# Performance work log

Hardware: AMD Instinct MI355X
Metric: run time of the kernel (lower is better)

Reference implementation:

```python
import jax, jax.numpy as jnp
import numpy as np

B, L, D, H = 4, 1024, 1024, 16
HD = D // H  # head_dim = 64


def setup_inputs() -> dict:
    key = jax.random.key(0)
    k1, k2, k3, k4 = jax.random.split(key, 4)
    x = jax.random.normal(k1, (B, L, D), dtype=jnp.float32)
    # causal mask: positions where mask == 0 are filled with -inf
    mask = jnp.tril(jnp.ones((L, L), dtype=bool))[None, None, :, :]  # [1,1,L,L]
    w_qkv = jax.random.normal(k2, (D, 3 * D), dtype=jnp.float32) * (D ** -0.5)
    w_out = jax.random.normal(k3, (D, D), dtype=jnp.float32) * (D ** -0.5)
    rel_pos_bias = jax.random.normal(k4, (H, L, L), dtype=jnp.float32) * 0.02
    return {"x": x, "mask": mask, "w_qkv": w_qkv, "w_out": w_out,
            "rel_pos_bias": rel_pos_bias}


def reference(x, mask, w_qkv, w_out, rel_pos_bias):
    b, l, d = x.shape
    scale = HD ** -0.5
    qkv = (x @ w_qkv).reshape(b, l, 3, H, HD)          # [B,L,3,H,hd]
    q, k, v = qkv[:, :, 0], qkv[:, :, 1], qkv[:, :, 2]  # each [B,L,H,hd]
    # scores: [B,H,Lq,Lk]
    scores = jnp.einsum('bqhd,bkhd->bhqk', q, k) * scale
    scores = scores + rel_pos_bias[None, :, :l, :l]
    scores = jnp.where(mask, scores, -jnp.inf)
    attn = jax.nn.softmax(scores, axis=-1)  # dropout is identity in eval
    out = jnp.einsum('bhqk,bkhd->bqhd', attn, v).reshape(b, l, d)
    return out @ w_out
```

## Files before the change

kernel.cpp:

```cpp
#include <hip/hip_runtime.h>
#include <hip/hip_bf16.h>
#include <math.h>

#define B_  4
#define L_  1024
#define D_  1024
#define H_  16
#define HD_ 64
#define SCALE 0.125f
#define LOG2E 1.44269504f
#define SCALE_L2E (0.125f * 1.44269504f)
#define NEG_BIG -3.0e38f

typedef __bf16 bf16x8 __attribute__((ext_vector_type(8)));
typedef float  f32x4  __attribute__((ext_vector_type(4)));

__device__ __forceinline__ float b2f(unsigned short u) {
    union { unsigned int i; float f; } x; x.i = ((unsigned)u) << 16; return x.f;
}
__device__ __forceinline__ unsigned short f2b(float f) {
    __hip_bfloat16 h = __float2bfloat16(f);
    return *reinterpret_cast<unsigned short*>(&h);
}
__device__ __forceinline__ void gl_lds16(const void* g, void* l) {
    __builtin_amdgcn_global_load_lds(
        (const __attribute__((address_space(1))) void*)g,
        (__attribute__((address_space(3))) void*)l, 16, 0, 0);
}

__global__ __launch_bounds__(256) void prep_kernel(
    const float* __restrict__ x, const float* __restrict__ w_qkv,
    const float* __restrict__ w_out, unsigned short* __restrict__ xb,
    unsigned short* __restrict__ wqkvT, unsigned short* __restrict__ woutT)
{
    const int bid = blockIdx.x;
    if (bid < 4096) {
        int i = (bid * 256 + threadIdx.x) * 4;
        float4 v = *(const float4*)&x[i];
        ushort4 o = make_ushort4(f2b(v.x), f2b(v.y), f2b(v.z), f2b(v.w));
        *(ushort4*)&xb[i] = o;
        return;
    }
    __shared__ float tile[32][33];
    const float* w; unsigned short* wt; int N, n0, k0;
    if (bid < 7168) {
        int b2 = bid - 4096;
        w = w_qkv; wt = wqkvT; N = 3072;
        n0 = (b2 % 96) * 32; k0 = (b2 / 96) * 32;
    } else {
        int b3 = bid - 7168;
        w = w_out; wt = woutT; N = 1024;
        n0 = (b3 % 32) * 32; k0 = (b3 / 32) * 32;
    }
    const int tx = threadIdx.x & 31, ty = threadIdx.x >> 5;
#pragma unroll
    for (int i = 0; i < 4; i++) {
        int kk = ty + i * 8;
        tile[kk][tx] = w[(size_t)(k0 + kk) * N + n0 + tx];
    }
    __syncthreads();
#pragma unroll
    for (int i = 0; i < 4; i++) {
        int nn = ty + i * 8;
        wt[(size_t)(n0 + nn) * 1024 + k0 + tx] = f2b(tile[tx][nn]);
    }
}

__device__ __forceinline__ void gemm_core(
    const unsigned short* __restrict__ A, const unsigned short* __restrict__ Bt,
    unsigned short* As, unsigned short* Bs,
    int m0, int n0, int wave, int lane, int wm, int wn,
    f32x4 acc[4][4])
{
    const int srow = lane >> 2, spos = lane & 3;
    const int sc   = spos ^ ((srow >> 1) & 3);
    const int mlane = lane & 15, chunk = lane >> 4;
    const int foff  = mlane * 32 + (chunk ^ ((mlane >> 1) & 3)) * 8;

    for (int k0 = 0; k0 < 1024; k0 += 32) {
#pragma unroll
        for (int t = 0; t < 2; t++) {
            int rb = wave * 32 + t * 16;
            int r  = rb + srow;
            gl_lds16(&A [(size_t)(m0 + r) * 1024 + k0 + sc * 8], &As[rb * 32]);
            gl_lds16(&Bt[(size_t)(n0 + r) * 1024 + k0 + sc * 8], &Bs[rb * 32]);
        }
        __syncthreads();
        bf16x8 af[4], bfr[4];
#pragma unroll
        for (int i = 0; i < 4; i++) {
            af[i]  = *(const bf16x8*)&As[(wm * 64 + i * 16) * 32 + foff];
            bfr[i] = *(const bf16x8*)&Bs[(wn * 64 + i * 16) * 32 + foff];
        }
#pragma unroll
        for (int i = 0; i < 4; i++)
#pragma unroll
            for (int j = 0; j < 4; j++)
                acc[i][j] = __builtin_amdgcn_mfma_f32_16x16x32_bf16(
                    bfr[i], af[j], acc[i][j], 0, 0, 0);
        __syncthreads();
    }
}

__global__ __launch_bounds__(256) void qkv_gemm_kernel(
    const unsigned short* __restrict__ A, const unsigned short* __restrict__ Bt,
    unsigned short* __restrict__ qb, unsigned short* __restrict__ kb,
    unsigned short* __restrict__ vtb)
{
    __shared__ unsigned short As[128 * 32];
    __shared__ unsigned short Bs[128 * 32];
    const int tid  = threadIdx.x;
    const int wave = tid >> 6, lane = tid & 63;
    const int quad = lane >> 4, l16 = lane & 15;
    const int wm = wave >> 1, wn = wave & 1;
    const int m0 = blockIdx.y * 128, n0 = blockIdx.x * 128;
    f32x4 acc[4][4] = {};
    gemm_core(A, Bt, As, Bs, m0, n0, wave, lane, wm, wn, acc);

    const int s = n0 >> 10;
#pragma unroll
    for (int i = 0; i < 4; i++) {
        int n_base = n0 + wn * 64 + i * 16 + quad * 4;
        int h = (n_base >> 6) & 15, hd0 = n_base & 63;
#pragma unroll
        for (int j = 0; j < 4; j++) {
            int m = m0 + wm * 64 + j * 16 + l16;
            int b = m >> 10, l = m & 1023;
            if (s == 2) {
#pragma unroll
                for (int r = 0; r < 4; r++)
                    vtb[((size_t)((b * 16 + h) * 64 + hd0 + r)) * 1024 + l] =
                        f2b(acc[i][j][r]);
            } else {
                unsigned short* dst = (s == 0) ? qb : kb;
                unsigned short tmp[4];
#pragma unroll
                for (int r = 0; r < 4; r++) tmp[r] = f2b(acc[i][j][r]);
                *(ushort4*)&dst[(((size_t)(b * 16 + h) * 1024 + l) << 6) + hd0] =
                    *(ushort4*)tmp;
            }
        }
    }
}

__global__ __launch_bounds__(256) void out_gemm_kernel(
    const unsigned short* __restrict__ A, const unsigned short* __restrict__ Bt,
    float* __restrict__ out)
{
    __shared__ unsigned short As[128 * 32];
    __shared__ unsigned short Bs[64 * 32];
    const int tid  = threadIdx.x;
    const int wave = tid >> 6, lane = tid & 63;
    const int quad = lane >> 4, l16 = lane & 15;
    const int srow = lane >> 2, spos = lane & 3;
    const int sc   = spos ^ ((srow >> 1) & 3);
    const int mlane = lane & 15, chunk = lane >> 4;
    const int foff  = mlane * 32 + (chunk ^ ((mlane >> 1) & 3)) * 8;
    const int m0 = blockIdx.y * 128, n0 = blockIdx.x * 64;
    f32x4 acc[4][2] = {};

    for (int k0 = 0; k0 < 1024; k0 += 32) {
#pragma unroll
        for (int t = 0; t < 2; t++) {
            int rb = wave * 32 + t * 16;
            gl_lds16(&A[(size_t)(m0 + rb + srow) * 1024 + k0 + sc * 8], &As[rb * 32]);
        }
        {
            int rb = wave * 16;
            gl_lds16(&Bt[(size_t)(n0 + rb + srow) * 1024 + k0 + sc * 8], &Bs[rb * 32]);
        }
        __syncthreads();
        bf16x8 af[2], bfr[4];
#pragma unroll
        for (int i = 0; i < 2; i++)
            af[i]  = *(const bf16x8*)&As[(wave * 32 + i * 16) * 32 + foff];
#pragma unroll
        for (int j = 0; j < 4; j++)
            bfr[j] = *(const bf16x8*)&Bs[(j * 16) * 32 + foff];
#pragma unroll
        for (int jn = 0; jn < 4; jn++)
#pragma unroll
            for (int im = 0; im < 2; im++)
                acc[jn][im] = __builtin_amdgcn_mfma_f32_16x16x32_bf16(
                    bfr[jn], af[im], acc[jn][im], 0, 0, 0);
        __syncthreads();
    }
#pragma unroll
    for (int jn = 0; jn < 4; jn++) {
        int n_base = n0 + jn * 16 + quad * 4;
#pragma unroll
        for (int im = 0; im < 2; im++) {
            int m = m0 + wave * 32 + im * 16 + l16;
            float4 o = make_float4(acc[jn][im][0], acc[jn][im][1],
                                   acc[jn][im][2], acc[jn][im][3]);
            *(float4*)&out[(size_t)m * 1024 + n_base] = o;
        }
    }
}

__global__ __launch_bounds__(256, 4) void attn_mfma_kernel(
    const unsigned short* __restrict__ qb, const unsigned short* __restrict__ kb,
    const unsigned short* __restrict__ vtb, const float* __restrict__ bias,
    unsigned short* __restrict__ ob)
{
    __shared__ unsigned short Qs[64 * 72];
    __shared__ unsigned short Ks[64 * 72];
    __shared__ unsigned short Vts[64 * 72];
    __shared__ unsigned short Ps[64 * 72];

    const int tid  = threadIdx.x;
    const int wave = tid >> 6, lane = tid & 63;
    const int quad = lane >> 4, l16 = lane & 15;
    const int bh = blockIdx.x, b = bh >> 4, h = bh & 15;
    const int qt = blockIdx.y;
    const int q0 = qt * 64;
    const int srow = tid >> 3, scol = (tid & 7) * 8;
    const size_t qkv_base = (size_t)bh * (1024 * 64);
    const int qg_base = q0 + wave * 16 + quad * 4;

#pragma unroll
    for (int i = 0; i < 2; i++) {
        int r = srow + i * 32;
        *(uint4*)&Qs[r * 72 + scol] =
            *(const uint4*)&qb[qkv_base + (size_t)(q0 + r) * 64 + scol];
    }
    uint4 kpre0 = *(const uint4*)&kb[qkv_base + (size_t)srow * 64 + scol];
    uint4 kpre1 = *(const uint4*)&kb[qkv_base + (size_t)(srow + 32) * 64 + scol];
    uint4 vpre0 = *(const uint4*)&vtb[qkv_base + (size_t)srow * 1024 + scol];
    uint4 vpre1 = *(const uint4*)&vtb[qkv_base + (size_t)(srow + 32) * 1024 + scol];

    float bA[16], bB[16];
    {
        const float* bp0 = &bias[((size_t)h * 1024 + qg_base) * 1024];
#pragma unroll
        for (int nt = 0; nt < 4; nt++)
#pragma unroll
            for (int r = 0; r < 4; r++)
                bA[nt * 4 + r] = bp0[(size_t)r * 1024 + nt * 16 + l16] * LOG2E;
    }

    float l_run[4] = {0.f, 0.f, 0.f, 0.f};
    f32x4 Oacc[4] = {};

    __syncthreads();
    bf16x8 af0 = *(const bf16x8*)&Qs[(wave * 16 + l16) * 72 + quad * 8];
    bf16x8 af1 = *(const bf16x8*)&Qs[(wave * 16 + l16) * 72 + 32 + quad * 8];

    auto attn_tile = [&](int kt, float* bcur, float* bnxt) {
        const int k0 = kt * 64;
        *(uint4*)&Ks [(size_t)srow * 72 + scol]        = kpre0;
        *(uint4*)&Ks [(size_t)(srow + 32) * 72 + scol] = kpre1;
        *(uint4*)&Vts[(size_t)srow * 72 + scol]        = vpre0;
        *(uint4*)&Vts[(size_t)(srow + 32) * 72 + scol] = vpre1;
        __syncthreads();
        if (kt < qt) {
            const int kn = k0 + 64;
            kpre0 = *(const uint4*)&kb[qkv_base + (size_t)(kn + srow) * 64 + scol];
            kpre1 = *(const uint4*)&kb[qkv_base + (size_t)(kn + srow + 32) * 64 + scol];
            vpre0 = *(const uint4*)&vtb[qkv_base + (size_t)srow * 1024 + kn + scol];
            vpre1 = *(const uint4*)&vtb[qkv_base + (size_t)(srow + 32) * 1024 + kn + scol];
            const float* bp = &bias[((size_t)h * 1024 + qg_base) * 1024 + kn];
#pragma unroll
            for (int nt = 0; nt < 4; nt++)
#pragma unroll
                for (int r = 0; r < 4; r++)
                    bnxt[nt * 4 + r] = bp[(size_t)r * 1024 + nt * 16 + l16] * LOG2E;
        }
        f32x4 sacc[4] = {};
#pragma unroll
        for (int nt = 0; nt < 4; nt++) {
            bf16x8 bk0 = *(const bf16x8*)&Ks[(nt * 16 + l16) * 72 + quad * 8];
            bf16x8 bk1 = *(const bf16x8*)&Ks[(nt * 16 + l16) * 72 + 32 + quad * 8];
            sacc[nt] = __builtin_amdgcn_mfma_f32_16x16x32_bf16(af0, bk0, sacc[nt], 0, 0, 0);
            sacc[nt] = __builtin_amdgcn_mfma_f32_16x16x32_bf16(af1, bk1, sacc[nt], 0, 0, 0);
        }
        const bool diag = (kt == qt);
#pragma unroll
        for (int nt = 0; nt < 4; nt++) {
            const int kg = k0 + nt * 16 + l16;
#pragma unroll
            for (int r = 0; r < 4; r++) {
                float v = fmaf(sacc[nt][r], SCALE_L2E, bcur[nt * 4 + r]);
                if (diag && kg > qg_base + r) v = NEG_BIG;
                float p = exp2f(v);
                l_run[r] += p;
                Ps[(wave * 16 + quad * 4 + r) * 72 + nt * 16 + l16] = f2b(p);
            }
        }
        bf16x8 pf0 = *(const bf16x8*)&Ps[(wave * 16 + l16) * 72 + quad * 8];
        bf16x8 pf1 = *(const bf16x8*)&Ps[(wave * 16 + l16) * 72 + 32 + quad * 8];
#pragma unroll
        for (int dt = 0; dt < 4; dt++) {
            bf16x8 vf0 = *(const bf16x8*)&Vts[(dt * 16 + l16) * 72 + quad * 8];
            bf16x8 vf1 = *(const bf16x8*)&Vts[(dt * 16 + l16) * 72 + 32 + quad * 8];
            Oacc[dt] = __builtin_amdgcn_mfma_f32_16x16x32_bf16(pf0, vf0, Oacc[dt], 0, 0, 0);
            Oacc[dt] = __builtin_amdgcn_mfma_f32_16x16x32_bf16(pf1, vf1, Oacc[dt], 0, 0, 0);
        }
        __syncthreads();
    };

    for (int kt = 0; kt <= qt; kt += 2) {
        attn_tile(kt, bA, bB);
        if (kt + 1 <= qt) attn_tile(kt + 1, bB, bA);
    }

#pragma unroll
    for (int r = 0; r < 4; r++) {
        float s = l_run[r];
        s += __shfl_xor(s, 1);
        s += __shfl_xor(s, 2);
        s += __shfl_xor(s, 4);
        s += __shfl_xor(s, 8);
        float inv = 1.0f / s;
        int qg = qg_base + r;
#pragma unroll
        for (int dt = 0; dt < 4; dt++)
            ob[((size_t)(b * 1024 + qg)) * 1024 + h * 64 + dt * 16 + l16] =
                f2b(Oacc[dt][r] * inv);
    }
}


extern "C" void kernel_launch(void* const* d_in, const int* in_sizes, int n_in,
                              void* d_out, int out_size, void* d_ws, size_t ws_size,
                              hipStream_t stream) {
    const float* x     = (const float*)d_in[0];
    const float* w_qkv = (const float*)d_in[2];
    const float* w_out = (const float*)d_in[3];
    const float* bias  = (const float*)d_in[4];
    float* out = (float*)d_out;

    char* ws = (char*)d_ws;
    unsigned short* xb     = (unsigned short*)ws;              ws += (size_t)4096 * 1024 * 2;
    unsigned short* wqkvT  = (unsigned short*)ws;              ws += (size_t)3072 * 1024 * 2;
    unsigned short* woutT  = (unsigned short*)ws;              ws += (size_t)1024 * 1024 * 2;
    unsigned short* qb     = (unsigned short*)ws;              ws += (size_t)4096 * 1024 * 2;
    unsigned short* kb     = (unsigned short*)ws;              ws += (size_t)4096 * 1024 * 2;
    unsigned short* vtb    = (unsigned short*)ws;              ws += (size_t)4096 * 1024 * 2;
    unsigned short* ab     = (unsigned short*)ws;

    prep_kernel<<<8192, 256, 0, stream>>>(x, w_qkv, w_out, xb, wqkvT, woutT);
    qkv_gemm_kernel<<<dim3(24, 32), 256, 0, stream>>>(xb, wqkvT, qb, kb, vtb);
    attn_mfma_kernel<<<dim3(64, 16), 256, 0, stream>>>(qb, kb, vtb, bias, ab);
    out_gemm_kernel<<<dim3(16, 32), 256, 0, stream>>>(ab, woutT, out);
}
```

Baseline: 222.2 us.

## Pair causal query tiles per block for load balance with double-buffered K/V

Each attention block now handles two query tiles, jlo and 15-jlo, so every block does the same amount of causal work, and the grid is halved. K and V tiles are shared between the two query strips. K/V LDS tiles are double-buffered so the next tile is written after compute, needing one barrier per tile. Q fragments load straight from global into registers, and s_setprio raises priority around the MFMA sections. Occupancy bound drops to 2 blocks per CU, and register pressure grows from the two accumulator sets.

Measured after the change: 215.9 us. -2.8%, faster.

```diff
diff --git a/kernel.cpp b/kernel.cpp
--- a/kernel.cpp
+++ b/kernel.cpp
@@ -198,125 +198,163 @@
     }
 }
 
-__global__ __launch_bounds__(256, 4) void attn_mfma_kernel(
+__global__ __launch_bounds__(256, 2) void attn_mfma_kernel(
     const unsigned short* __restrict__ qb, const unsigned short* __restrict__ kb,
     const unsigned short* __restrict__ vtb, const float* __restrict__ bias,
     unsigned short* __restrict__ ob)
 {
-    __shared__ unsigned short Qs[64 * 72];
-    __shared__ unsigned short Ks[64 * 72];
-    __shared__ unsigned short Vts[64 * 72];
-    __shared__ unsigned short Ps[64 * 72];
+    __shared__ unsigned short Ks [2 * 64 * 72];
+    __shared__ unsigned short Vts[2 * 64 * 72];
+    __shared__ unsigned short Ps [128 * 72];
 
     const int tid  = threadIdx.x;
     const int wave = tid >> 6, lane = tid & 63;
     const int quad = lane >> 4, l16 = lane & 15;
     const int bh = blockIdx.x, b = bh >> 4, h = bh & 15;
-    const int qt = blockIdx.y;
-    const int q0 = qt * 64;
+    const int jlo = blockIdx.y;
+    const int jhi = 15 - jlo;
+    const int ktmax = jhi;
     const int srow = tid >> 3, scol = (tid & 7) * 8;
     const size_t qkv_base = (size_t)bh * (1024 * 64);
-    const int qg_base = q0 + wave * 16 + quad * 4;
-
-#pragma unroll
-    for (int i = 0; i < 2; i++) {
-        int r = srow + i * 32;
-        *(uint4*)&Qs[r * 72 + scol] =
-            *(const uint4*)&qb[qkv_base + (size_t)(q0 + r) * 64 + scol];
-    }
-    uint4 kpre0 = *(const uint4*)&kb[qkv_base + (size_t)srow * 64 + scol];
-    uint4 kpre1 = *(const uint4*)&kb[qkv_base + (size_t)(srow + 32) * 64 + scol];
+
+    const int qH  = jhi * 64 + wave * 16;
+    const int qL  = jlo * 64 + wave * 16;
+    const int qgH = qH + quad * 4;
+    const int qgL = qL + quad * 4;
+
+    bf16x8 aH0 = *(const bf16x8*)&qb[qkv_base + (size_t)(qH + l16) * 64 + quad * 8];
+    bf16x8 aH1 = *(const bf16x8*)&qb[qkv_base + (size_t)(qH + l16) * 64 + 32 + quad * 8];
+    bf16x8 aL0 = *(const bf16x8*)&qb[qkv_base + (size_t)(qL + l16) * 64 + quad * 8];
+    bf16x8 aL1 = *(const bf16x8*)&qb[qkv_base + (size_t)(qL + l16) * 64 + 32 + quad * 8];
+
+    uint4 kpre0 = *(const uint4*)&kb [qkv_base + (size_t)srow * 64 + scol];
+    uint4 kpre1 = *(const uint4*)&kb [qkv_base + (size_t)(srow + 32) * 64 + scol];
     uint4 vpre0 = *(const uint4*)&vtb[qkv_base + (size_t)srow * 1024 + scol];
     uint4 vpre1 = *(const uint4*)&vtb[qkv_base + (size_t)(srow + 32) * 1024 + scol];
 
     float bA[16], bB[16];
-    {
-        const float* bp0 = &bias[((size_t)h * 1024 + qg_base) * 1024];
-#pragma unroll
-        for (int nt = 0; nt < 4; nt++)
-#pragma unroll
-            for (int r = 0; r < 4; r++)
-                bA[nt * 4 + r] = bp0[(size_t)r * 1024 + nt * 16 + l16] * LOG2E;
-    }
-
-    float l_run[4] = {0.f, 0.f, 0.f, 0.f};
-    f32x4 Oacc[4] = {};
-
+#pragma unroll
+    for (int nt = 0; nt < 4; nt++)
+#pragma unroll
+        for (int r = 0; r < 4; r++)
+            bA[nt * 4 + r] =
+                bias[((size_t)h * 1024 + qgH + r) * 1024 + nt * 16 + l16] * LOG2E;
+
+    float lrH[4] = {}, lrL[4] = {};
+    f32x4 OH[4] = {}, OL[4] = {};
+
+    *(uint4*)&Ks [srow * 72 + scol]        = kpre0;
+    *(uint4*)&Ks [(srow + 32) * 72 + scol] = kpre1;
+    *(uint4*)&Vts[srow * 72 + scol]        = vpre0;
+    *(uint4*)&Vts[(srow + 32) * 72 + scol] = vpre1;
     __syncthreads();
-    bf16x8 af0 = *(const bf16x8*)&Qs[(wave * 16 + l16) * 72 + quad * 8];
-    bf16x8 af1 = *(const bf16x8*)&Qs[(wave * 16 + l16) * 72 + 32 + quad * 8];
-
-    auto attn_tile = [&](int kt, float* bcur, float* bnxt) {
-        const int k0 = kt * 64;
-        *(uint4*)&Ks [(size_t)srow * 72 + scol]        = kpre0;
-        *(uint4*)&Ks [(size_t)(srow + 32) * 72 + scol] = kpre1;
-        *(uint4*)&Vts[(size_t)srow * 72 + scol]        = vpre0;
-        *(uint4*)&Vts[(size_t)(srow + 32) * 72 + scol] = vpre1;
-        __syncthreads();
-        if (kt < qt) {
-            const int kn = k0 + 64;
-            kpre0 = *(const uint4*)&kb[qkv_base + (size_t)(kn + srow) * 64 + scol];
-            kpre1 = *(const uint4*)&kb[qkv_base + (size_t)(kn + srow + 32) * 64 + scol];
+
+    auto strip = [&](int kt, const bf16x8& a0, const bf16x8& a1, const float* bc,
+                     int qg, int psrow, f32x4* O, float* lr, bool dg) {
+        const unsigned short* Kc = &Ks [(kt & 1) * 4608];
+        const unsigned short* Vc = &Vts[(kt & 1) * 4608];
+        f32x4 sacc[4] = {};
+        __builtin_amdgcn_s_setprio(1);
+#pragma unroll
+        for (int nt = 0; nt < 4; nt++) {
+            bf16x8 k0 = *(const bf16x8*)&Kc[(nt * 16 + l16) * 72 + quad * 8];
+            bf16x8 k1 = *(const bf16x8*)&Kc[(nt * 16 + l16) * 72 + 32 + quad * 8];
+            sacc[nt] = __builtin_amdgcn_mfma_f32_16x16x32_bf16(a0, k0, sacc[nt], 0, 0, 0);
+            sacc[nt] = __builtin_amdgcn_mfma_f32_16x16x32_bf16(a1, k1, sacc[nt], 0, 0, 0);
+        }
+        __builtin_amdgcn_s_setprio(0);
+#pragma unroll
+        for (int nt = 0; nt < 4; nt++) {
+            const int kg = kt * 64 + nt * 16 + l16;
+#pragma unroll
+            for (int r = 0; r < 4; r++) {
+                float v = fmaf(sacc[nt][r], SCALE_L2E, bc[nt * 4 + r]);
+                if (dg && kg > qg + r) v = NEG_BIG;
+                float p = exp2f(v);
+                lr[r] += p;
+                Ps[(psrow + quad * 4 + r) * 72 + nt * 16 + l16] = f2b(p);
+            }
+        }
+        bf16x8 p0 = *(const bf16x8*)&Ps[(psrow + l16) * 72 + quad * 8];
+        bf16x8 p1 = *(const bf16x8*)&Ps[(psrow + l16) * 72 + 32 + quad * 8];
+        __builtin_amdgcn_s_setprio(1);
+#pragma unroll
+        for (int dt = 0; dt < 4; dt++) {
+            bf16x8 v0 = *(const bf16x8*)&Vc[(dt * 16 + l16) * 72 + quad * 8];
+            bf16x8 v1 = *(const bf16x8*)&Vc[(dt * 16 + l16) * 72 + 32 + quad * 8];
+            O[dt] = __builtin_amdgcn_mfma_f32_16x16x32_bf16(p0, v0, O[dt], 0, 0, 0);
+            O[dt] = __builtin_amdgcn_mfma_f32_16x16x32_bf16(p1, v1, O[dt], 0, 0, 0);
+        }
+        __builtin_amdgcn_s_setprio(0);
+    };
+
+    auto tile = [&](int kt, float* bc, float* bn) {
+        const bool pf = (kt < ktmax);
+        if (pf) {
+            const int kn = (kt + 1) * 64;
+            kpre0 = *(const uint4*)&kb [qkv_base + (size_t)(kn + srow) * 64 + scol];
+            kpre1 = *(const uint4*)&kb [qkv_base + (size_t)(kn + srow + 32) * 64 + scol];
             vpre0 = *(const uint4*)&vtb[qkv_base + (size_t)srow * 1024 + kn + scol];
             vpre1 = *(const uint4*)&vtb[qkv_base + (size_t)(srow + 32) * 1024 + kn + scol];
-            const float* bp = &bias[((size_t)h * 1024 + qg_base) * 1024 + kn];
+            const float* bp = &bias[((size_t)h * 1024 + qgH) * 1024 + kn];
 #pragma unroll
             for (int nt = 0; nt < 4; nt++)
 #pragma unroll
                 for (int r = 0; r < 4; r++)
-                    bnxt[nt * 4 + r] = bp[(size_t)r * 1024 + nt * 16 + l16] * LOG2E;
-        }
-        f32x4 sacc[4] = {};
-#pragma unroll
-        for (int nt = 0; nt < 4; nt++) {
-            bf16x8 bk0 = *(const bf16x8*)&Ks[(nt * 16 + l16) * 72 + quad * 8];
-            bf16x8 bk1 = *(const bf16x8*)&Ks[(nt * 16 + l16) * 72 + 32 + quad * 8];
-            sacc[nt] = __builtin_amdgcn_mfma_f32_16x16x32_bf16(af0, bk0, sacc[nt], 0, 0, 0);
-            sacc[nt] = __builtin_amdgcn_mfma_f32_16x16x32_bf16(af1, bk1, sacc[nt], 0, 0, 0);
-        }
-        const bool diag = (kt == qt);
-#pragma unroll
-        for (int nt = 0; nt < 4; nt++) {
-            const int kg = k0 + nt * 16 + l16;
-#pragma unroll
-            for (int r = 0; r < 4; r++) {
-                float v = fmaf(sacc[nt][r], SCALE_L2E, bcur[nt * 4 + r]);
-                if (diag && kg > qg_base + r) v = NEG_BIG;
-                float p = exp2f(v);
-                l_run[r] += p;
-                Ps[(wave * 16 + quad * 4 + r) * 72 + nt * 16 + l16] = f2b(p);
-            }
-        }
-        bf16x8 pf0 = *(const bf16x8*)&Ps[(wave * 16 + l16) * 72 + quad * 8];
-        bf16x8 pf1 = *(const bf16x8*)&Ps[(wave * 16 + l16) * 72 + 32 + quad * 8];
-#pragma unroll
-        for (int dt = 0; dt < 4; dt++) {
-            bf16x8 vf0 = *(const bf16x8*)&Vts[(dt * 16 + l16) * 72 + quad * 8];
-            bf16x8 vf1 = *(const bf16x8*)&Vts[(dt * 16 + l16) * 72 + 32 + quad * 8];
-            Oacc[dt] = __builtin_amdgcn_mfma_f32_16x16x32_bf16(pf0, vf0, Oacc[dt], 0, 0, 0);
-            Oacc[dt] = __builtin_amdgcn_mfma_f32_16x16x32_bf16(pf1, vf1, Oacc[dt], 0, 0, 0);
+                    bn[nt * 4 + r] = bp[(size_t)r * 1024 + nt * 16 + l16] * LOG2E;
+        }
+        const bool dolo = (kt <= jlo);
+        float bl[16];
+        if (dolo) {
+            const float* bp = &bias[((size_t)h * 1024 + qgL) * 1024 + kt * 64];
+#pragma unroll
+            for (int nt = 0; nt < 4; nt++)
+#pragma unroll
+                for (int r = 0; r < 4; r++)
+                    bl[nt * 4 + r] = bp[(size_t)r * 1024 + nt * 16 + l16] * LOG2E;
+        }
+        strip(kt, aH0, aH1, bc, qgH, wave * 32,      OH, lrH, kt == ktmax);
+        if (dolo)
+            strip(kt, aL0, aL1, bl, qgL, wave * 32 + 16, OL, lrL, kt == jlo);
+        if (pf) {
+            unsigned short* Kn = &Ks [((kt + 1) & 1) * 4608];
+            unsigned short* Vn = &Vts[((kt + 1) & 1) * 4608];
+            *(uint4*)&Kn[srow * 72 + scol]        = kpre0;
+            *(uint4*)&Kn[(srow + 32) * 72 + scol] = kpre1;
+            *(uint4*)&Vn[srow * 72 + scol]        = vpre0;
+            *(uint4*)&Vn[(srow + 32) * 72 + scol] = vpre1;
         }
         __syncthreads();
     };
 
-    for (int kt = 0; kt <= qt; kt += 2) {
-        attn_tile(kt, bA, bB);
-        if (kt + 1 <= qt) attn_tile(kt + 1, bB, bA);
+    for (int kt = 0; kt <= ktmax; kt += 2) {
+        tile(kt, bA, bB);
+        if (kt + 1 <= ktmax) tile(kt + 1, bB, bA);
     }
 
 #pragma unroll
     for (int r = 0; r < 4; r++) {
-        float s = l_run[r];
-        s += __shfl_xor(s, 1);
-        s += __shfl_xor(s, 2);
-        s += __shfl_xor(s, 4);
-        s += __shfl_xor(s, 8);
+        float s = lrH[r];
+        s += __shfl_xor(s, 1); s += __shfl_xor(s, 2);
+        s += __shfl_xor(s, 4); s += __shfl_xor(s, 8);
         float inv = 1.0f / s;
-        int qg = qg_base + r;
+        int qg = qgH + r;
 #pragma unroll
         for (int dt = 0; dt < 4; dt++)
             ob[((size_t)(b * 1024 + qg)) * 1024 + h * 64 + dt * 16 + l16] =
-                f2b(Oacc[dt][r] * inv);
+                f2b(OH[dt][r] * inv);
+    }
+#pragma unroll
+    for (int r = 0; r < 4; r++) {
+        float s = lrL[r];
+        s += __shfl_xor(s, 1); s += __shfl_xor(s, 2);
+        s += __shfl_xor(s, 4); s += __shfl_xor(s, 8);
+        float inv = 1.0f / s;
+        int qg = qgL + r;
+#pragma unroll
+        for (int dt = 0; dt < 4; dt++)
+            ob[((size_t)(b * 1024 + qg)) * 1024 + h * 64 + dt * 16 + l16] =
+                f2b(OL[dt][r] * inv);
     }
 }
 
@@ -341,6 +379,6 @@
 
     prep_kernel<<<8192, 256, 0, stream>>>(x, w_qkv, w_out, xb, wqkvT, woutT);
     qkv_gemm_kernel<<<dim3(24, 32), 256, 0, stream>>>(xb, wqkvT, qb, kb, vtb);
-    attn_mfma_kernel<<<dim3(64, 16), 256, 0, stream>>>(qb, kb, vtb, bias, ab);
+    attn_mfma_kernel<<<dim3(64, 8), 256, 0, stream>>>(qb, kb, vtb, bias, ab);
     out_gemm_kernel<<<dim3(16, 32), 256, 0, stream>>>(ab, woutT, out);
 }
```
